# Performance work log

Measured on AMD Instinct MI355X. Metric: run time of the kernel, lower is better.

## Reference

```python
import jax, jax.numpy as jnp
import numpy as np

HEAD_DIM = 32
KERNEL = 3
DILATION = 2
SCALE = HEAD_DIM ** -0.5


def _unfold(x, kernel, dilation):
    # x: [B, C, H, W] -> patches [B, C, kernel*kernel, H, W]
    # matches nn.Unfold(kernel, dilation, padding=dilation*(kernel-1)//2, stride=1)
    B, C, H, W = x.shape
    pad = dilation * (kernel - 1) // 2
    xp = jnp.pad(x, ((0, 0), (0, 0), (pad, pad), (pad, pad)))
    patches = jnp.stack(
        [xp[:, :, i * dilation:i * dilation + H, j * dilation:j * dilation + W]
         for i in range(kernel) for j in range(kernel)],
        axis=2,
    )
    return patches  # [B, C, k*k, H, W]


def setup_inputs() -> dict:
    key = jax.random.key(0)
    kq, kk, kv = jax.random.split(key, 3)
    shape = (8, 192, 56, 56)
    return {
        "q": jax.random.normal(kq, shape, dtype=jnp.float32),
        "k": jax.random.normal(kk, shape, dtype=jnp.float32),
        "v": jax.random.normal(kv, shape, dtype=jnp.float32),
    }


def reference(q, k, v):
    B, d, H, W = q.shape
    h = d // HEAD_DIM
    kk2 = KERNEL * KERNEL
    HW = H * W

    # q: [B, h, hd, HW]
    qh = q.reshape(B, h, HEAD_DIM, HW)
    # unfolded k/v: [B, h, hd, k*k, HW]
    kp = _unfold(k, KERNEL, DILATION).reshape(B, h, HEAD_DIM, kk2, HW)
    vp = _unfold(v, KERNEL, DILATION).reshape(B, h, HEAD_DIM, kk2, HW)

    attn = jnp.einsum('bhdn,bhdkn->bhnk', qh, kp) * SCALE
    attn = jax.nn.softmax(attn, axis=-1)
    # dropout p=0 (eval): no-op

    # [B, h, HW, hd]
    out = jnp.einsum('bhnk,bhdkn->bhnd', attn, vp)
    # transpose(1,2).reshape(B,H,W,d): channel order = head-major
    out = out.transpose(0, 2, 1, 3).reshape(B, H, W, d)
    return out
```

## Files before the change

kernel.cpp:

```cpp
#include <hip/hip_runtime.h>

#define NH 6
#define HEAD_DIM 32
#define CCH 192
#define HH 56
#define WW 56
#define HWSZ (HH * WW)
#define KPOS 9
#define SCALE 0.17677669529663687f
#define XPAD 61
#define ROWSZ (HEAD_DIM * XPAD)
#define JROWS 4
#define STRIPS 7

__global__ __launch_bounds__(256, 4) void dilate_attn_roll(
    const float* __restrict__ q,
    const float* __restrict__ k,
    const float* __restrict__ v,
    float* __restrict__ out)
{
    __shared__ float ks[3][ROWSZ];
    __shared__ float vs[3][ROWSZ];

    const int bh     = blockIdx.x % 48;
    const int ps     = blockIdx.x / 48;
    const int parity = ps / STRIPS;
    const int s      = ps % STRIPS;
    const int y0     = parity + 8 * s;
    const int t      = threadIdx.x;

    const size_t plane = (size_t)bh * HEAD_DIM * HWSZ;
    const int px = t >> 2;
    const int c  = t & 3;
    const bool active = px < WW;

    int sd[7], sx[7];
#pragma unroll
    for (int i = 0; i < 7; i++) {
        const int e = t + 256 * i;
        sd[i] = e / WW;
        sx[i] = e - sd[i] * WW;
    }

    float qcur[8];
    if (active) {
        const float* qb = q + plane + (size_t)(8 * c) * HWSZ + (size_t)y0 * WW + px;
#pragma unroll
        for (int j = 0; j < 8; j++) qcur[j] = qb[j * HWSZ];
    }

    for (int e = t; e < 3 * HEAD_DIM * 4; e += 256) {
        const int slot = e >> 7;
        const int rr   = e & 127;
        const int d    = rr >> 2;
        const int xc   = rr & 3;
        const int xp   = (xc < 2) ? xc : (56 + xc);
        ks[slot][d * XPAD + xp] = 0.0f;
        vs[slot][d * XPAD + xp] = 0.0f;
    }

    float kpre[7], vpre[7];
#pragma unroll
    for (int r = 0; r < 3; r++) {
        const int ky   = y0 - 2 + 2 * r;
        const bool okr = (ky >= 0) && (ky < HH);
#pragma unroll
        for (int i = 0; i < 7; i++) {
            const size_t g = plane + (size_t)sd[i] * HWSZ + (size_t)(okr ? ky : 0) * WW + sx[i];
            kpre[i] = okr ? k[g] : 0.0f;
            vpre[i] = okr ? v[g] : 0.0f;
        }
#pragma unroll
        for (int i = 0; i < 7; i++) {
            const int a = sd[i] * XPAD + sx[i] + 2;
            ks[r][a] = kpre[i];
            vs[r][a] = vpre[i];
        }
    }
    __syncthreads();

    float qnxt[8];
#pragma unroll
    for (int j = 0; j < JROWS; j++) {
        const int y = y0 + 2 * j;

        if (j < 3) {
            const int ky   = y0 + 4 + 2 * j;
            const bool okr = (ky < HH);
#pragma unroll
            for (int i = 0; i < 7; i++) {
                const size_t g = plane + (size_t)sd[i] * HWSZ + (size_t)(okr ? ky : 0) * WW + sx[i];
                kpre[i] = okr ? k[g] : 0.0f;
                vpre[i] = okr ? v[g] : 0.0f;
            }
            if (active) {
                const float* qb = q + plane + (size_t)(8 * c) * HWSZ + (size_t)(y + 2) * WW + px;
#pragma unroll
                for (int jj = 0; jj < 8; jj++) qnxt[jj] = qb[jj * HWSZ];
            }
        }

        if (active) {
            float lg[KPOS];
#pragma unroll
            for (int rp = 0; rp < 3; rp++) {
                const float* kr = &ks[(j + rp) % 3][(8 * c) * XPAD + px];
                float a0 = 0.f, a1 = 0.f, a2 = 0.f;
#pragma unroll
                for (int j8 = 0; j8 < 8; j8++) {
                    const float* p  = kr + j8 * XPAD;
                    const float qj = qcur[j8];
                    a0 = fmaf(qj, p[0], a0);
                    a1 = fmaf(qj, p[2], a1);
                    a2 = fmaf(qj, p[4], a2);
                }
                lg[3 * rp + 0] = a0;
                lg[3 * rp + 1] = a1;
                lg[3 * rp + 2] = a2;
            }
#pragma unroll
            for (int kk = 0; kk < KPOS; kk++) {
                float sm = lg[kk];
                sm += __shfl_xor(sm, 1);
                sm += __shfl_xor(sm, 2);
                lg[kk] = sm * SCALE;
            }
            float m = lg[0];
#pragma unroll
            for (int kk = 1; kk < KPOS; kk++) m = fmaxf(m, lg[kk]);
            float ssum = 0.f;
#pragma unroll
            for (int kk = 0; kk < KPOS; kk++) {
                lg[kk] = __expf(lg[kk] - m);
                ssum += lg[kk];
            }
            const float inv = 1.f / ssum;

            float acc[8];
#pragma unroll
            for (int jj = 0; jj < 8; jj++) acc[jj] = 0.f;
#pragma unroll
            for (int rp = 0; rp < 3; rp++) {
                const float* vr = &vs[(j + rp) % 3][(8 * c) * XPAD + px];
                const float w0 = lg[3 * rp + 0] * inv;
                const float w1 = lg[3 * rp + 1] * inv;
                const float w2 = lg[3 * rp + 2] * inv;
#pragma unroll
                for (int jj = 0; jj < 8; jj++) {
                    const float* p = vr + jj * XPAD;
                    float a = acc[jj];
                    a = fmaf(w0, p[0], a);
                    a = fmaf(w1, p[2], a);
                    a = fmaf(w2, p[4], a);
                    acc[jj] = a;
                }
            }

            const int h = bh % NH;
            const int b = bh / NH;
            float* ob = out + ((size_t)((b * HH + y) * WW + px)) * CCH
                            + h * HEAD_DIM + 8 * c;
            reinterpret_cast<float4*>(ob)[0] = make_float4(acc[0], acc[1], acc[2], acc[3]);
            reinterpret_cast<float4*>(ob)[1] = make_float4(acc[4], acc[5], acc[6], acc[7]);
        }

        __syncthreads();

        if (j < 3) {
#pragma unroll
            for (int i = 0; i < 7; i++) {
                const int a = sd[i] * XPAD + sx[i] + 2;
                ks[j % 3][a] = kpre[i];
                vs[j % 3][a] = vpre[i];
            }
#pragma unroll
            for (int jj = 0; jj < 8; jj++) qcur[jj] = qnxt[jj];
        }

        __syncthreads();
    }
}

extern "C" void kernel_launch(void* const* d_in, const int* in_sizes, int n_in,
                              void* d_out, int out_size, void* d_ws, size_t ws_size,
                              hipStream_t stream) {
    const float* q = (const float*)d_in[0];
    const float* k = (const float*)d_in[1];
    const float* v = (const float*)d_in[2];
    float* out = (float*)d_out;

    const int blocks = 48 * 2 * STRIPS;
    dilate_attn_roll<<<blocks, 256, 0, stream>>>(q, k, v, out);
}
```

Before: 105.6 us.

## Split each pixel's head dimension across eight lanes with 512-thread blocks

Doubles the block size to 512 threads so each pixel is handled by 8 lanes, each holding 4 channels instead of 8. A third shuffle stage is added to the logit reduction. The three initial K/V row loads are issued together before any shared-memory store, and the trailing barriers after the last row are dropped. The intent is to raise per-block parallelism and memory-level parallelism with fewer registers per thread, at the cost of extra shuffles and more idle threads in the final load pass.

```diff
diff --git a/kernel.cpp b/kernel.cpp
--- a/kernel.cpp
+++ b/kernel.cpp
@@ -12,8 +12,10 @@
 #define ROWSZ (HEAD_DIM * XPAD)
 #define JROWS 4
 #define STRIPS 7
-
-__global__ __launch_bounds__(256, 4) void dilate_attn_roll(
+#define NT 512
+#define SELEMS (HEAD_DIM * WW)
+
+__global__ __launch_bounds__(NT, 6) void dilate_attn_roll8(
     const float* __restrict__ q,
     const float* __restrict__ k,
     const float* __restrict__ v,
@@ -30,28 +32,31 @@
     const int t      = threadIdx.x;
 
     const size_t plane = (size_t)bh * HEAD_DIM * HWSZ;
-    const int px = t >> 2;
-    const int c  = t & 3;
+    const int px = t >> 3;
+    const int c  = t & 7;
     const bool active = px < WW;
 
-    int sd[7], sx[7];
-#pragma unroll
-    for (int i = 0; i < 7; i++) {
-        const int e = t + 256 * i;
-        sd[i] = e / WW;
-        sx[i] = e - sd[i] * WW;
-    }
-
-    float qcur[8];
+    int sd[4], sx[4];
+    bool sv[4];
+#pragma unroll
+    for (int i = 0; i < 4; i++) {
+        const int e = t + NT * i;
+        sv[i] = (e < SELEMS);
+        const int ee = sv[i] ? e : 0;
+        sd[i] = ee / WW;
+        sx[i] = ee - sd[i] * WW;
+    }
+
+    float qcur[4];
     if (active) {
-        const float* qb = q + plane + (size_t)(8 * c) * HWSZ + (size_t)y0 * WW + px;
-#pragma unroll
-        for (int j = 0; j < 8; j++) qcur[j] = qb[j * HWSZ];
-    }
-
-    for (int e = t; e < 3 * HEAD_DIM * 4; e += 256) {
-        const int slot = e >> 7;
-        const int rr   = e & 127;
+        const float* qb = q + plane + (size_t)(4 * c) * HWSZ + (size_t)y0 * WW + px;
+#pragma unroll
+        for (int d = 0; d < 4; d++) qcur[d] = qb[d * HWSZ];
+    }
+
+    if (t < 3 * HEAD_DIM * 4) {
+        const int slot = t >> 7;
+        const int rr   = t & 127;
         const int d    = rr >> 2;
         const int xc   = rr & 3;
         const int xp   = (xc < 2) ? xc : (56 + xc);
@@ -59,44 +64,55 @@
         vs[slot][d * XPAD + xp] = 0.0f;
     }
 
-    float kpre[7], vpre[7];
+    float kp[3][4], vp[3][4];
 #pragma unroll
     for (int r = 0; r < 3; r++) {
         const int ky   = y0 - 2 + 2 * r;
-        const bool okr = (ky >= 0) && (ky < HH);
-#pragma unroll
-        for (int i = 0; i < 7; i++) {
-            const size_t g = plane + (size_t)sd[i] * HWSZ + (size_t)(okr ? ky : 0) * WW + sx[i];
-            kpre[i] = okr ? k[g] : 0.0f;
-            vpre[i] = okr ? v[g] : 0.0f;
-        }
-#pragma unroll
-        for (int i = 0; i < 7; i++) {
-            const int a = sd[i] * XPAD + sx[i] + 2;
-            ks[r][a] = kpre[i];
-            vs[r][a] = vpre[i];
+        const bool okr = ((unsigned)ky < HH);
+        const float* kb = k + plane + (size_t)(okr ? ky : 0) * WW;
+        const float* vb = v + plane + (size_t)(okr ? ky : 0) * WW;
+#pragma unroll
+        for (int i = 0; i < 4; i++) {
+            const size_t g = (size_t)sd[i] * HWSZ + sx[i];
+            const bool ok  = okr && sv[i];
+            kp[r][i] = ok ? kb[g] : 0.0f;
+            vp[r][i] = ok ? vb[g] : 0.0f;
+        }
+    }
+#pragma unroll
+    for (int r = 0; r < 3; r++) {
+#pragma unroll
+        for (int i = 0; i < 4; i++) {
+            if (sv[i]) {
+                const int a = sd[i] * XPAD + sx[i] + 2;
+                ks[r][a] = kp[r][i];
+                vs[r][a] = vp[r][i];
+            }
         }
     }
     __syncthreads();
 
-    float qnxt[8];
+    float qnxt[4], kn[4], vn[4];
 #pragma unroll
     for (int j = 0; j < JROWS; j++) {
         const int y = y0 + 2 * j;
 
-        if (j < 3) {
+        if (j < JROWS - 1) {
             const int ky   = y0 + 4 + 2 * j;
             const bool okr = (ky < HH);
-#pragma unroll
-            for (int i = 0; i < 7; i++) {
-                const size_t g = plane + (size_t)sd[i] * HWSZ + (size_t)(okr ? ky : 0) * WW + sx[i];
-                kpre[i] = okr ? k[g] : 0.0f;
-                vpre[i] = okr ? v[g] : 0.0f;
+            const float* kb = k + plane + (size_t)(okr ? ky : 0) * WW;
+            const float* vb = v + plane + (size_t)(okr ? ky : 0) * WW;
+#pragma unroll
+            for (int i = 0; i < 4; i++) {
+                const size_t g = (size_t)sd[i] * HWSZ + sx[i];
+                const bool ok  = okr && sv[i];
+                kn[i] = ok ? kb[g] : 0.0f;
+                vn[i] = ok ? vb[g] : 0.0f;
             }
             if (active) {
-                const float* qb = q + plane + (size_t)(8 * c) * HWSZ + (size_t)(y + 2) * WW + px;
-#pragma unroll
-                for (int jj = 0; jj < 8; jj++) qnxt[jj] = qb[jj * HWSZ];
+                const float* qb = q + plane + (size_t)(4 * c) * HWSZ + (size_t)(y + 2) * WW + px;
+#pragma unroll
+                for (int d = 0; d < 4; d++) qnxt[d] = qb[d * HWSZ];
             }
         }
 
@@ -104,15 +120,15 @@
             float lg[KPOS];
 #pragma unroll
             for (int rp = 0; rp < 3; rp++) {
-                const float* kr = &ks[(j + rp) % 3][(8 * c) * XPAD + px];
+                const float* kr = &ks[(j + rp) % 3][(4 * c) * XPAD + px];
                 float a0 = 0.f, a1 = 0.f, a2 = 0.f;
 #pragma unroll
-                for (int j8 = 0; j8 < 8; j8++) {
-                    const float* p  = kr + j8 * XPAD;
-                    const float qj = qcur[j8];
-                    a0 = fmaf(qj, p[0], a0);
-                    a1 = fmaf(qj, p[2], a1);
-                    a2 = fmaf(qj, p[4], a2);
+                for (int d = 0; d < 4; d++) {
+                    const float* p  = kr + d * XPAD;
+                    const float qd = qcur[d];
+                    a0 = fmaf(qd, p[0], a0);
+                    a1 = fmaf(qd, p[2], a1);
+                    a2 = fmaf(qd, p[4], a2);
                 }
                 lg[3 * rp + 0] = a0;
                 lg[3 * rp + 1] = a1;
@@ -123,6 +139,7 @@
                 float sm = lg[kk];
                 sm += __shfl_xor(sm, 1);
                 sm += __shfl_xor(sm, 2);
+                sm += __shfl_xor(sm, 4);
                 lg[kk] = sm * SCALE;
             }
             float m = lg[0];
@@ -136,48 +153,47 @@
             }
             const float inv = 1.f / ssum;
 
-            float acc[8];
-#pragma unroll
-            for (int jj = 0; jj < 8; jj++) acc[jj] = 0.f;
+            float acc[4] = {0.f, 0.f, 0.f, 0.f};
 #pragma unroll
             for (int rp = 0; rp < 3; rp++) {
-                const float* vr = &vs[(j + rp) % 3][(8 * c) * XPAD + px];
+                const float* vr = &vs[(j + rp) % 3][(4 * c) * XPAD + px];
                 const float w0 = lg[3 * rp + 0] * inv;
                 const float w1 = lg[3 * rp + 1] * inv;
                 const float w2 = lg[3 * rp + 2] * inv;
 #pragma unroll
-                for (int jj = 0; jj < 8; jj++) {
-                    const float* p = vr + jj * XPAD;
-                    float a = acc[jj];
+                for (int d = 0; d < 4; d++) {
+                    const float* p = vr + d * XPAD;
+                    float a = acc[d];
                     a = fmaf(w0, p[0], a);
                     a = fmaf(w1, p[2], a);
                     a = fmaf(w2, p[4], a);
-                    acc[jj] = a;
+                    acc[d] = a;
                 }
             }
 
             const int h = bh % NH;
             const int b = bh / NH;
             float* ob = out + ((size_t)((b * HH + y) * WW + px)) * CCH
-                            + h * HEAD_DIM + 8 * c;
-            reinterpret_cast<float4*>(ob)[0] = make_float4(acc[0], acc[1], acc[2], acc[3]);
-            reinterpret_cast<float4*>(ob)[1] = make_float4(acc[4], acc[5], acc[6], acc[7]);
-        }
-
-        __syncthreads();
-
-        if (j < 3) {
-#pragma unroll
-            for (int i = 0; i < 7; i++) {
-                const int a = sd[i] * XPAD + sx[i] + 2;
-                ks[j % 3][a] = kpre[i];
-                vs[j % 3][a] = vpre[i];
-            }
-#pragma unroll
-            for (int jj = 0; jj < 8; jj++) qcur[jj] = qnxt[jj];
-        }
-
-        __syncthreads();
+                            + h * HEAD_DIM + 4 * c;
+            *reinterpret_cast<float4*>(ob) = make_float4(acc[0], acc[1], acc[2], acc[3]);
+        }
+
+        if (j < JROWS - 1) {
+            __syncthreads();
+
+#pragma unroll
+            for (int i = 0; i < 4; i++) {
+                if (sv[i]) {
+                    const int a = sd[i] * XPAD + sx[i] + 2;
+                    ks[j % 3][a] = kn[i];
+                    vs[j % 3][a] = vn[i];
+                }
+            }
+#pragma unroll
+            for (int d = 0; d < 4; d++) qcur[d] = qnxt[d];
+
+            __syncthreads();
+        }
     }
 }
 
@@ -190,5 +206,5 @@
     float* out = (float*)d_out;
 
     const int blocks = 48 * 2 * STRIPS;
-    dilate_attn_roll<<<blocks, 256, 0, stream>>>(q, k, v, out);
+    dilate_attn_roll8<<<blocks, NT, 0, stream>>>(q, k, v, out);
 }
```

Result: slower. 116.9 us (+10.7%).
